# Performance work log

Hardware: AMD Instinct MI355X
Metric: run time of the kernel (lower is better)

Reference implementation:

```python
import jax, jax.numpy as jnp
import numpy as np

RADIUS = 4
SIGMA1 = 5.0
SIGMA2 = 1.0


def _gauss_1d(radius, sigma):
    x = jnp.arange(-radius, radius + 1, dtype=jnp.float32)
    return jnp.exp(-(x ** 2) / (2.0 * sigma ** 2))  # peak-1 gaussian (norm.pdf(d)/norm.pdf(0))


def _blur3d(x, g, radius):
    # Separable 3D gaussian conv; product of 1D kernels == exp(-(dx^2+dy^2+dz^2)/(2*sigma^2)),
    # mathematically identical to the dense (2r+1)^3 conv3d in the torch module.
    dn = ('NCDHW', 'OIDHW', 'NCDHW')
    for ax in range(3):
        shape = [1, 1, 1, 1, 1]
        shape[2 + ax] = g.shape[0]
        k = g.reshape(shape)
        pad = [(0, 0), (0, 0), (0, 0)]
        pad[ax] = (radius, radius)
        x = jax.lax.conv_general_dilated(x, k, (1, 1, 1), pad, dimension_numbers=dn)
    return x


def setup_inputs() -> dict:
    key = jax.random.key(0)
    k1, k2 = jax.random.split(key)
    labels = jax.random.uniform(k1, (2, 4, 128, 128, 128), dtype=jnp.float32)
    inputs = jax.random.normal(k2, (2, 1, 128, 128, 128), dtype=jnp.float32)
    return {"labels": labels, "inputs": inputs}


def reference(labels, inputs):
    num_classes = labels.shape[1]
    g = _gauss_1d(RADIUS, SIGMA1)
    loss = jnp.float32(0.0)
    for k in range(num_classes):
        class_probs = labels[:, k:k + 1]  # [B,1,D,H,W]
        class_mean = (jnp.mean(inputs * class_probs, axis=(2, 3, 4), keepdims=True)
                      / (jnp.mean(class_probs, axis=(2, 3, 4), keepdims=True) + 1e-5))  # [B,C,1,1,1]
        diff = jnp.sum((inputs - class_mean) ** 2, axis=1, keepdims=True)  # [B,1,D,H,W]
        weights = jnp.exp(-(diff ** 2) / (SIGMA2 ** 2))
        numerator = jnp.sum(class_probs * _blur3d(class_probs * weights, g, RADIUS))
        denominator = jnp.sum(class_probs * _blur3d(weights, g, RADIUS))
        # L1Loss(x, 0) on a scalar == |x|
        loss = loss + jnp.abs(numerator / (denominator + 1e-6))
    return num_classes - loss
```

## Files before the change

kernel.cpp:

```cpp
#include <hip/hip_runtime.h>
#include <math.h>

#define DIM   128
#define SLICE (DIM*DIM)
#define VOL   (DIM*DIM*DIM)
#define NK    4
#define NVOL  8
#define SSTR  33

__constant__ float c_g[9] = {
    0.72614904f, 0.83527021f, 0.92311635f, 0.98019867f, 1.0f,
    0.98019867f, 0.92311635f, 0.83527021f, 0.72614904f
};

__device__ __forceinline__ void lds_barrier() {
    __builtin_amdgcn_s_waitcnt(0xC07F);
    __builtin_amdgcn_s_barrier();
}


__global__ __launch_bounds__(256) void k_sums(
    const float* __restrict__ labels, const float* __restrict__ inputs,
    float* __restrict__ partials)
{
    const int b     = blockIdx.x >> 9;
    const int chunk = blockIdx.x & 511;
    const int t     = threadIdx.x;
    const size_t off4 = (size_t)chunk*1024 + t;
    const float4* __restrict__ I4 = (const float4*)inputs + (size_t)b*(VOL/4) + off4;
    const float4* __restrict__ L4 = (const float4*)labels;
    float sp[4] = {0,0,0,0}, sip[4] = {0,0,0,0};
    #pragma unroll
    for (int j = 0; j < 4; ++j) {
        const float4 iv = I4[j*256];
        #pragma unroll
        for (int k = 0; k < 4; ++k) {
            const float4 p = L4[(size_t)(b*NK + k)*(VOL/4) + off4 + j*256];
            sp[k]  += p.x + p.y + p.z + p.w;
            sip[k] += p.x*iv.x + p.y*iv.y + p.z*iv.z + p.w*iv.w;
        }
    }
    #pragma unroll
    for (int k = 0; k < 4; ++k) {
        #pragma unroll
        for (int o = 32; o; o >>= 1) {
            sp[k]  += __shfl_down(sp[k],  o);
            sip[k] += __shfl_down(sip[k], o);
        }
    }
    __shared__ float sB[8][4];
    const int wid = t >> 6;
    if ((t & 63) == 0) {
        #pragma unroll
        for (int k = 0; k < 4; ++k) { sB[k][wid] = sp[k]; sB[4+k][wid] = sip[k]; }
    }
    __syncthreads();
    if (t < 8) partials[blockIdx.x*8 + t] = sB[t][0] + sB[t][1] + sB[t][2] + sB[t][3];
}

__global__ void k_reduce(const float* __restrict__ partials, float* __restrict__ red)
{
    __shared__ float sB[16][16];
    const int t = threadIdx.x;
    const int s = t & 15;
    const int i = t >> 4;
    const int b = s >> 3, j = s & 7;
    float acc = 0.f;
    for (int c = i; c < 512; c += 16)
        acc += partials[(size_t)(b*512 + c)*8 + j];
    sB[s][i] = acc;
    __syncthreads();
    if (t < 16) {
        float v = 0.f;
        #pragma unroll
        for (int q = 0; q < 16; ++q) v += sB[t][q];
        const int bb = t >> 3, jj = t & 7;
        const int vol = bb*NK + (jj & 3);
        red[(jj < 4 ? vol : 8 + vol)] = v;
    }
}

__global__ __launch_bounds__(256, 4) void k_fused(
    const float* __restrict__ labels, const float* __restrict__ inputs,
    const float* __restrict__ red, float* __restrict__ nd)
{
    __shared__ float4 sW[2][16*SSTR + 8];
    __shared__ float sN[4], sD[4];

    const int dq    = blockIdx.x & 3;
    const int strip = (blockIdx.x >> 2) & 15;
    const int vol   = blockIdx.x >> 6;
    const int b = vol >> 2, kcls = vol & 3;
    const int d0 = dq * 32;
    const int t  = threadIdx.x;
    const float g1 = c_g[5], g2 = c_g[6], g3 = c_g[7], g4 = c_g[8];
    const float4 z4 = make_float4(0.f, 0.f, 0.f, 0.f);

    const float* __restrict__ src = labels + (size_t)vol*VOL;
    const float mean = red[8+vol] / (red[vol] + 20.97152f);

    const int r0 = t >> 5, c0 = t & 31;
    const int r1 = r0 + 8;
    const int ho = t >> 5, wq = t & 31;

    const int hA = strip*8 - 4 + r0;
    const int hB = strip*8 - 4 + r1;
    const bool vA = (unsigned)hA < 128u;
    const bool vB = (unsigned)hB < 128u;
    const float4* __restrict__ rowA = (const float4*)(src + (size_t)(vA ? hA : 0)*DIM);
    const float4* __restrict__ rowB = (const float4*)(src + (size_t)(vB ? hB : 0)*DIM);

    const size_t ob4 = (size_t)(strip*8 + ho)*(DIM/4) + wq;
    const float4* __restrict__ P4 = (const float4*)src + ob4;
    const float4* __restrict__ I4 = (const float4*)(inputs + (size_t)b*VOL) + ob4;

    float4 ring[9];
    #pragma unroll
    for (int i = 0; i < 9; ++i) ring[i] = z4;
    float numAcc = 0.f, denAcc = 0.f;

    auto ldA = [&](int s, float4& pv, float4& cv, float4& nx) {
        pv = cv = nx = z4;
        if (vA && (unsigned)s < 128u) {
            const float4* rp = rowA + (size_t)s*(SLICE/4);
            cv = rp[c0];
            if (c0 > 0)  pv = rp[c0-1];
            if (c0 < 31) nx = rp[c0+1];
        }
    };
    auto ldB = [&](int s, float4& pv, float4& cv, float4& nx) {
        pv = cv = nx = z4;
        if (vB && (unsigned)s < 128u) {
            const float4* rp = rowB + (size_t)s*(SLICE/4);
            cv = rp[c0];
            if (c0 > 0)  pv = rp[c0-1];
            if (c0 < 31) nx = rp[c0+1];
        }
    };

    float4 Apv, Acv, Anx, Bpv, Bcv, Bnx;
    ldA(d0-4, Apv, Acv, Anx);
    ldB(d0-4, Bpv, Bcv, Bnx);

    #pragma unroll 2
    for (int s = d0-4; s < d0+36; ++s) {
        const float4 apv=Apv, acv=Acv, anx=Anx, bpv=Bpv, bcv=Bcv, bnx=Bnx;
        ldA(s+1, Apv, Acv, Anx);
        ldB(s+1, Bpv, Bcv, Bnx);
        float4 pc = z4, ic = z4;
        const bool outStep = (s >= d0+4);
        if (outStep) {
            pc = P4[(size_t)(s-4)*(SLICE/4)];
            ic = I4[(size_t)(s-4)*(SLICE/4)];
        }
        const int buf = s & 1;
        {
            float4 o;
            o.x = acv.x + g1*(apv.w+acv.y) + g2*(apv.z+acv.z) + g3*(apv.y+acv.w) + g4*(apv.x+anx.x);
            o.y = acv.y + g1*(acv.x+acv.z) + g2*(apv.w+acv.w) + g3*(apv.z+anx.x) + g4*(apv.y+anx.y);
            o.z = acv.z + g1*(acv.y+acv.w) + g2*(acv.x+anx.x) + g3*(apv.w+anx.y) + g4*(apv.z+anx.z);
            o.w = acv.w + g1*(acv.z+anx.x) + g2*(acv.y+anx.y) + g3*(acv.x+anx.z) + g4*(apv.w+anx.w);
            sW[buf][r0*SSTR + c0] = o;
        }
        {
            float4 o;
            o.x = bcv.x + g1*(bpv.w+bcv.y) + g2*(bpv.z+bcv.z) + g3*(bpv.y+bcv.w) + g4*(bpv.x+bnx.x);
            o.y = bcv.y + g1*(bcv.x+bcv.z) + g2*(bpv.w+bcv.w) + g3*(bpv.z+bnx.x) + g4*(bpv.y+bnx.y);
            o.z = bcv.z + g1*(bcv.y+bcv.w) + g2*(bcv.x+bnx.x) + g3*(bpv.w+bnx.y) + g4*(bpv.z+bnx.z);
            o.w = bcv.w + g1*(bcv.z+bnx.x) + g2*(bcv.y+bnx.y) + g3*(bcv.x+bnx.z) + g4*(bpv.w+bnx.w);
            sW[buf][r1*SSTR + c0] = o;
        }
        lds_barrier();
        float4 acc = sW[buf][(ho+4)*SSTR + wq];
        #pragma unroll
        for (int dt = 1; dt <= 4; ++dt) {
            const float g = c_g[4+dt];
            const float4 u = sW[buf][(ho+4-dt)*SSTR + wq];
            const float4 v = sW[buf][(ho+4+dt)*SSTR + wq];
            acc.x += g*(u.x+v.x); acc.y += g*(u.y+v.y);
            acc.z += g*(u.z+v.z); acc.w += g*(u.w+v.w);
        }
        #pragma unroll
        for (int i = 0; i < 8; ++i) ring[i] = ring[i+1];
        ring[8] = acc;
        if (outStep) {
            float4 B = ring[4];
            #pragma unroll
            for (int dt = 1; dt <= 4; ++dt) {
                const float g = c_g[4+dt];
                B.x += g*(ring[4+dt].x + ring[4-dt].x);
                B.y += g*(ring[4+dt].y + ring[4-dt].y);
                B.z += g*(ring[4+dt].z + ring[4-dt].z);
                B.w += g*(ring[4+dt].w + ring[4-dt].w);
            }
            { float df = ic.x - mean; df *= df; const float bw = B.x * __expf(-df*df); numAcc += bw*pc.x; denAcc += bw; }
            { float df = ic.y - mean; df *= df; const float bw = B.y * __expf(-df*df); numAcc += bw*pc.y; denAcc += bw; }
            { float df = ic.z - mean; df *= df; const float bw = B.z * __expf(-df*df); numAcc += bw*pc.z; denAcc += bw; }
            { float df = ic.w - mean; df *= df; const float bw = B.w * __expf(-df*df); numAcc += bw*pc.w; denAcc += bw; }
        }
    }

    #pragma unroll
    for (int o = 32; o; o >>= 1) { numAcc += __shfl_down(numAcc, o); denAcc += __shfl_down(denAcc, o); }
    if ((t & 63) == 0) { sN[t >> 6] = numAcc; sD[t >> 6] = denAcc; }
    __syncthreads();
    if (t == 0) {
        atomicAdd(&nd[kcls],   sN[0]+sN[1]+sN[2]+sN[3]);
        atomicAdd(&nd[4+kcls], sD[0]+sD[1]+sD[2]+sD[3]);
    }
}

__global__ void k_final(const float* __restrict__ red, float* __restrict__ out)
{
    float loss = 0.f;
    #pragma unroll
    for (int k = 0; k < 4; ++k) loss += fabsf(red[16+k] / (red[20+k] + 1e-6f));
    out[0] = (float)NK - loss;
}

extern "C" void kernel_launch(void* const* d_in, const int* in_sizes, int n_in,
                              void* d_out, int out_size, void* d_ws, size_t ws_size,
                              hipStream_t stream)
{
    const float* labels = (const float*)d_in[0];
    const float* inputs = (const float*)d_in[1];
    float* out = (float*)d_out;
    float* red = (float*)d_ws;
    float* partials = red + 32;

    hipMemsetAsync(red + 16, 0, 8*sizeof(float), stream);
    k_sums<<<2*512, 256, 0, stream>>>(labels, inputs, partials);
    k_reduce<<<1, 256, 0, stream>>>(partials, red);
    k_fused<<<NVOL*16*4, 256, 0, stream>>>(labels, inputs, red, red + 16);
    k_final<<<1, 1, 0, stream>>>(red, out);
}
```

Measured before the change: 215.9 us.

## Use wavefront shuffles for W-halo and stagger class chunks in sums kernel

In the fused blur kernel, each thread now loads only its own float4 per row and gets the neighbouring float4s from adjacent lanes with shuffles. This replaces three global loads per row with one (lanes 0 and 31 zero-pad). The sums kernel doubles its grid to smaller chunks and XOR-staggers which chunk each class reads, so concurrent blocks hit different memory regions at the cost of extra inputs loads when chunks differ. The custom LDS barrier is swapped for __syncthreads.

```diff
diff --git a/kernel.cpp b/kernel.cpp
--- a/kernel.cpp
+++ b/kernel.cpp
@@ -13,9 +13,13 @@
     0.98019867f, 0.92311635f, 0.83527021f, 0.72614904f
 };
 
-__device__ __forceinline__ void lds_barrier() {
-    __builtin_amdgcn_s_waitcnt(0xC07F);
-    __builtin_amdgcn_s_barrier();
+__device__ __forceinline__ float4 shfl_up4(float4 v) {
+    return make_float4(__shfl_up(v.x,1), __shfl_up(v.y,1),
+                       __shfl_up(v.z,1), __shfl_up(v.w,1));
+}
+__device__ __forceinline__ float4 shfl_dn4(float4 v) {
+    return make_float4(__shfl_down(v.x,1), __shfl_down(v.y,1),
+                       __shfl_down(v.z,1), __shfl_down(v.w,1));
 }
 
 
@@ -23,21 +27,24 @@
     const float* __restrict__ labels, const float* __restrict__ inputs,
     float* __restrict__ partials)
 {
-    const int b     = blockIdx.x >> 9;
-    const int chunk = blockIdx.x & 511;
+    const int b     = blockIdx.x >> 10;
+    const int chunk = blockIdx.x & 1023;
     const int t     = threadIdx.x;
-    const size_t off4 = (size_t)chunk*1024 + t;
-    const float4* __restrict__ I4 = (const float4*)inputs + (size_t)b*(VOL/4) + off4;
     const float4* __restrict__ L4 = (const float4*)labels;
+    const float4* __restrict__ I4 = (const float4*)inputs + (size_t)b*(VOL/4);
     float sp[4] = {0,0,0,0}, sip[4] = {0,0,0,0};
     #pragma unroll
-    for (int j = 0; j < 4; ++j) {
-        const float4 iv = I4[j*256];
+    for (int j = 0; j < 2; ++j) {
+        const size_t oi = (size_t)chunk*512 + j*256 + t;
+        const float4 iv = I4[oi];
         #pragma unroll
         for (int k = 0; k < 4; ++k) {
-            const float4 p = L4[(size_t)(b*NK + k)*(VOL/4) + off4 + j*256];
+            const int ck = (chunk ^ (k*341)) & 1023;
+            const size_t ol = (size_t)ck*512 + j*256 + t;
+            const float4 p = L4[(size_t)(b*NK + k)*(VOL/4) + ol];
             sp[k]  += p.x + p.y + p.z + p.w;
-            sip[k] += p.x*iv.x + p.y*iv.y + p.z*iv.z + p.w*iv.w;
+            const float4 iv2 = (ck == chunk) ? iv : I4[ol];
+            sip[k] += p.x*iv2.x + p.y*iv2.y + p.z*iv2.z + p.w*iv2.w;
         }
     }
     #pragma unroll
@@ -66,8 +73,8 @@
     const int i = t >> 4;
     const int b = s >> 3, j = s & 7;
     float acc = 0.f;
-    for (int c = i; c < 512; c += 16)
-        acc += partials[(size_t)(b*512 + c)*8 + j];
+    for (int c = i; c < 1024; c += 16)
+        acc += partials[(size_t)(b*1024 + c)*8 + j];
     sB[s][i] = acc;
     __syncthreads();
     if (t < 16) {
@@ -107,8 +114,8 @@
     const int hB = strip*8 - 4 + r1;
     const bool vA = (unsigned)hA < 128u;
     const bool vB = (unsigned)hB < 128u;
-    const float4* __restrict__ rowA = (const float4*)(src + (size_t)(vA ? hA : 0)*DIM);
-    const float4* __restrict__ rowB = (const float4*)(src + (size_t)(vB ? hB : 0)*DIM);
+    const float4* __restrict__ rowA = (const float4*)(src + (size_t)(vA ? hA : 0)*DIM) + c0;
+    const float4* __restrict__ rowB = (const float4*)(src + (size_t)(vB ? hB : 0)*DIM) + c0;
 
     const size_t ob4 = (size_t)(strip*8 + ho)*(DIM/4) + wq;
     const float4* __restrict__ P4 = (const float4*)src + ob4;
@@ -119,34 +126,21 @@
     for (int i = 0; i < 9; ++i) ring[i] = z4;
     float numAcc = 0.f, denAcc = 0.f;
 
-    auto ldA = [&](int s, float4& pv, float4& cv, float4& nx) {
-        pv = cv = nx = z4;
-        if (vA && (unsigned)s < 128u) {
-            const float4* rp = rowA + (size_t)s*(SLICE/4);
-            cv = rp[c0];
-            if (c0 > 0)  pv = rp[c0-1];
-            if (c0 < 31) nx = rp[c0+1];
-        }
+    auto ldA = [&](int s) -> float4 {
+        return (vA && (unsigned)s < 128u) ? rowA[(size_t)s*(SLICE/4)] : z4;
     };
-    auto ldB = [&](int s, float4& pv, float4& cv, float4& nx) {
-        pv = cv = nx = z4;
-        if (vB && (unsigned)s < 128u) {
-            const float4* rp = rowB + (size_t)s*(SLICE/4);
-            cv = rp[c0];
-            if (c0 > 0)  pv = rp[c0-1];
-            if (c0 < 31) nx = rp[c0+1];
-        }
+    auto ldB = [&](int s) -> float4 {
+        return (vB && (unsigned)s < 128u) ? rowB[(size_t)s*(SLICE/4)] : z4;
     };
 
-    float4 Apv, Acv, Anx, Bpv, Bcv, Bnx;
-    ldA(d0-4, Apv, Acv, Anx);
-    ldB(d0-4, Bpv, Bcv, Bnx);
+    float4 Acv = ldA(d0-4);
+    float4 Bcv = ldB(d0-4);
 
     #pragma unroll 2
     for (int s = d0-4; s < d0+36; ++s) {
-        const float4 apv=Apv, acv=Acv, anx=Anx, bpv=Bpv, bcv=Bcv, bnx=Bnx;
-        ldA(s+1, Apv, Acv, Anx);
-        ldB(s+1, Bpv, Bcv, Bnx);
+        const float4 acv = Acv, bcv = Bcv;
+        Acv = ldA(s+1);
+        Bcv = ldB(s+1);
         float4 pc = z4, ic = z4;
         const bool outStep = (s >= d0+4);
         if (outStep) {
@@ -155,22 +149,26 @@
         }
         const int buf = s & 1;
         {
+            float4 pv = shfl_up4(acv); if (c0 == 0)  pv = z4;
+            float4 nx = shfl_dn4(acv); if (c0 == 31) nx = z4;
             float4 o;
-            o.x = acv.x + g1*(apv.w+acv.y) + g2*(apv.z+acv.z) + g3*(apv.y+acv.w) + g4*(apv.x+anx.x);
-            o.y = acv.y + g1*(acv.x+acv.z) + g2*(apv.w+acv.w) + g3*(apv.z+anx.x) + g4*(apv.y+anx.y);
-            o.z = acv.z + g1*(acv.y+acv.w) + g2*(acv.x+anx.x) + g3*(apv.w+anx.y) + g4*(apv.z+anx.z);
-            o.w = acv.w + g1*(acv.z+anx.x) + g2*(acv.y+anx.y) + g3*(acv.x+anx.z) + g4*(apv.w+anx.w);
+            o.x = acv.x + g1*(pv.w+acv.y) + g2*(pv.z+acv.z) + g3*(pv.y+acv.w) + g4*(pv.x+nx.x);
+            o.y = acv.y + g1*(acv.x+acv.z) + g2*(pv.w+acv.w) + g3*(pv.z+nx.x) + g4*(pv.y+nx.y);
+            o.z = acv.z + g1*(acv.y+acv.w) + g2*(acv.x+nx.x) + g3*(pv.w+nx.y) + g4*(pv.z+nx.z);
+            o.w = acv.w + g1*(acv.z+nx.x) + g2*(acv.y+nx.y) + g3*(acv.x+nx.z) + g4*(pv.w+nx.w);
             sW[buf][r0*SSTR + c0] = o;
         }
         {
+            float4 pv = shfl_up4(bcv); if (c0 == 0)  pv = z4;
+            float4 nx = shfl_dn4(bcv); if (c0 == 31) nx = z4;
             float4 o;
-            o.x = bcv.x + g1*(bpv.w+bcv.y) + g2*(bpv.z+bcv.z) + g3*(bpv.y+bcv.w) + g4*(bpv.x+bnx.x);
-            o.y = bcv.y + g1*(bcv.x+bcv.z) + g2*(bpv.w+bcv.w) + g3*(bpv.z+bnx.x) + g4*(bpv.y+bnx.y);
-            o.z = bcv.z + g1*(bcv.y+bcv.w) + g2*(bcv.x+bnx.x) + g3*(bpv.w+bnx.y) + g4*(bpv.z+bnx.z);
-            o.w = bcv.w + g1*(bcv.z+bnx.x) + g2*(bcv.y+bnx.y) + g3*(bcv.x+bnx.z) + g4*(bpv.w+bnx.w);
+            o.x = bcv.x + g1*(pv.w+bcv.y) + g2*(pv.z+bcv.z) + g3*(pv.y+bcv.w) + g4*(pv.x+nx.x);
+            o.y = bcv.y + g1*(bcv.x+bcv.z) + g2*(pv.w+bcv.w) + g3*(pv.z+nx.x) + g4*(pv.y+nx.y);
+            o.z = bcv.z + g1*(bcv.y+bcv.w) + g2*(bcv.x+nx.x) + g3*(pv.w+nx.y) + g4*(pv.z+nx.z);
+            o.w = bcv.w + g1*(bcv.z+nx.x) + g2*(bcv.y+nx.y) + g3*(bcv.x+nx.z) + g4*(pv.w+nx.w);
             sW[buf][r1*SSTR + c0] = o;
         }
-        lds_barrier();
+        __syncthreads();
         float4 acc = sW[buf][(ho+4)*SSTR + wq];
         #pragma unroll
         for (int dt = 1; dt <= 4; ++dt) {
@@ -229,7 +227,7 @@
     float* partials = red + 32;
 
     hipMemsetAsync(red + 16, 0, 8*sizeof(float), stream);
-    k_sums<<<2*512, 256, 0, stream>>>(labels, inputs, partials);
+    k_sums<<<2*1024, 256, 0, stream>>>(labels, inputs, partials);
     k_reduce<<<1, 256, 0, stream>>>(partials, red);
     k_fused<<<NVOL*16*4, 256, 0, stream>>>(labels, inputs, red, red + 16);
     k_final<<<1, 1, 0, stream>>>(red, out);
```

After: 221.0 us. 1.02x slower.
